# Kernel optimization log

Hardware: AMD Instinct MI355X
Metric: run time of the kernel (lower is better)

## Reference

```python
import jax, jax.numpy as jnp
import numpy as np

GROUPS = 32
EPS = 1e-3  # keras GroupNormalization default epsilon


def setup_inputs() -> dict:
    key = jax.random.key(0)
    ks = jax.random.split(key, 7)
    B, H, W, C = 16, 32, 32, 512
    inputs = jax.random.normal(ks[0], (B, H, W, C), dtype=jnp.float32)
    gamma = jnp.ones((C,), dtype=jnp.float32)
    beta = jnp.zeros((C,), dtype=jnp.float32)
    # EinsumDense 'bhwc,cae->bhwae', output last dims (C,3), bias axes 'ae'
    W_qkv = jax.random.normal(ks[1], (C, C, 3), dtype=jnp.float32) / np.sqrt(C)
    b_qkv = jnp.zeros((C, 3), dtype=jnp.float32)
    # EinsumDense 'bhwc,cd->bhwd', bias axes 'd'
    W_out = jax.random.normal(ks[2], (C, C), dtype=jnp.float32) / np.sqrt(C)
    b_out = jnp.zeros((C,), dtype=jnp.float32)
    return {
        "inputs": inputs,
        "gamma": gamma,
        "beta": beta,
        "W_qkv": W_qkv,
        "b_qkv": b_qkv,
        "W_out": W_out,
        "b_out": b_out,
    }


def group_norm(x, gamma, beta):
    B, H, W, C = x.shape
    g = GROUPS
    xr = x.reshape(B, H, W, g, C // g)
    mean = jnp.mean(xr, axis=(1, 2, 4), keepdims=True)
    var = jnp.var(xr, axis=(1, 2, 4), keepdims=True)
    xn = (xr - mean) * jax.lax.rsqrt(var + EPS)
    return xn.reshape(B, H, W, C) * gamma + beta


def reference(inputs, gamma, beta, W_qkv, b_qkv, W_out, b_out):
    B, H, W, C = inputs.shape
    scale = C ** (-0.5)
    x = group_norm(inputs, gamma, beta)
    # QKV projection: bhwc,cae->bhwae  (+ bias over 'ae')
    qkv = jnp.einsum("bhwc,cae->bhwae", x, W_qkv) + b_qkv
    q, k, v = qkv[..., 0], qkv[..., 1], qkv[..., 2]  # each [B,H,W,C]
    # full spatial attention: [B,H,W,H,W]
    attn = jnp.einsum("bhwc,btlc->bhwtl", q, k) * scale
    attn = attn.reshape(B, H, W, H * W)
    attn = jax.nn.softmax(attn, axis=-1)
    attn = attn.reshape(B, H, W, H, W)
    out = jnp.einsum("bhwtl,btlc->bhwc", attn, v)
    out = jnp.einsum("bhwc,cd->bhwd", out, W_out) + b_out
    return inputs + out
```

## Files before the change

### kernel.cpp

```cpp
#include <hip/hip_runtime.h>
#include <hip/hip_bf16.h>

#define NB    16
#define SP    1024
#define NC    512
#define NG    32
#define MTOT  (NB*SP)
#define EPSV  1e-3f
#define SCALE 0.04419417382415922f

using f32x4   = __attribute__((ext_vector_type(4))) float;
using short8  = __attribute__((ext_vector_type(8))) short;
using short4v = __attribute__((ext_vector_type(4))) short;
using bf16x8v = __attribute__((ext_vector_type(8))) __bf16;

__device__ __forceinline__ unsigned short f2bf(float f) {
  union { float f; unsigned int u; } x; x.f = f;
  unsigned int u = x.u;
  unsigned int r = (u + 0x7FFFu + ((u >> 16) & 1u)) >> 16;
  return (unsigned short)r;
}
__device__ __forceinline__ float bf2f(unsigned short b) {
  union { unsigned int u; float f; } x; x.u = ((unsigned int)b) << 16;
  return x.f;
}

#define GLOAD_LDS16(g, l)                                                     \
  __builtin_amdgcn_global_load_lds(                                           \
      (const __attribute__((address_space(1))) void*)(g),                     \
      (__attribute__((address_space(3))) void*)(l), 16, 0, 0)

__global__ __launch_bounds__(256) void gn_stats_k(const float* __restrict__ x,
                                                  float2* __restrict__ stats) {
  int bg = blockIdx.x;
  int b = bg >> 5, g = bg & 31;
  int tid = threadIdx.x;
  int c = tid & 15, s0 = tid >> 4;
  const float* base = x + (long)b * SP * NC + g * 16 + c;
  float s = 0.f, ss = 0.f;
  for (int sp = s0; sp < SP; sp += 16) {
    float v = base[(long)sp * NC];
    s += v; ss += v * v;
  }
  for (int o = 32; o > 0; o >>= 1) { s += __shfl_xor(s, o); ss += __shfl_xor(ss, o); }
  __shared__ float rs[4], rss[4];
  int lane = tid & 63, wv = tid >> 6;
  if (lane == 0) { rs[wv] = s; rss[wv] = ss; }
  __syncthreads();
  if (tid == 0) {
    float S = rs[0] + rs[1] + rs[2] + rs[3];
    float SS = rss[0] + rss[1] + rss[2] + rss[3];
    float mean = S * (1.f / 16384.f);
    float var  = SS * (1.f / 16384.f) - mean * mean;
    stats[bg] = make_float2(mean, rsqrtf(var + EPSV));
  }
}

__global__ __launch_bounds__(256) void gn_apply_k(const float* __restrict__ x,
                                                  const float2* __restrict__ stats,
                                                  const float* __restrict__ gamma,
                                                  const float* __restrict__ beta,
                                                  unsigned short* __restrict__ xn) {
  long t = (long)blockIdx.x * 256 + threadIdx.x;
  long base = t * 8;
  int c = (int)(base & 511);
  int b = (int)(base >> 19);
  float2 st = stats[b * NG + (c >> 4)];
  f32x4 v0 = *reinterpret_cast<const f32x4*>(x + base);
  f32x4 v1 = *reinterpret_cast<const f32x4*>(x + base + 4);
  f32x4 g0 = *reinterpret_cast<const f32x4*>(gamma + c);
  f32x4 g1 = *reinterpret_cast<const f32x4*>(gamma + c + 4);
  f32x4 b0 = *reinterpret_cast<const f32x4*>(beta + c);
  f32x4 b1 = *reinterpret_cast<const f32x4*>(beta + c + 4);
  short8 o;
  #pragma unroll
  for (int q = 0; q < 4; ++q) {
    float sc = st.y * g0[q];
    o[q] = (short)f2bf(v0[q] * sc + (b0[q] - st.x * sc));
  }
  #pragma unroll
  for (int q = 0; q < 4; ++q) {
    float sc = st.y * g1[q];
    o[q + 4] = (short)f2bf(v1[q] * sc + (b1[q] - st.x * sc));
  }
  *reinterpret_cast<short8*>(xn + base) = o;
}

__global__ __launch_bounds__(256) void pack_wqkv_k(const float* __restrict__ W,
                                                   const float* __restrict__ bq,
                                                   unsigned short* __restrict__ Wp,
                                                   float* __restrict__ bp) {
  int idx = blockIdx.x * 256 + threadIdx.x;
  int n = idx >> 9, c = idx & 511;
  int e = n >> 9, a = n & 511;
  Wp[idx] = f2bf(W[((long)c * 512 + a) * 3 + e]);
  if (idx < 1536) {
    int e2 = idx >> 9, a2 = idx & 511;
    bp[idx] = bq[a2 * 3 + e2];
  }
}

__global__ __launch_bounds__(256) void pack_wout_k(const float* __restrict__ W,
                                                   unsigned short* __restrict__ Wp) {
  int idx = blockIdx.x * 256 + threadIdx.x;
  int n = idx >> 9, c = idx & 511;
  Wp[idx] = f2bf(W[(long)c * 512 + n]);
}

__global__ void transpose_v_k(const unsigned short* __restrict__ qkv,
                              unsigned short* __restrict__ vT) {
  __shared__ unsigned short t[32][33];
  int bs = blockIdx.x, bc = blockIdx.y, b = blockIdx.z;
  int tx = threadIdx.x, ty = threadIdx.y;
  #pragma unroll
  for (int k = 0; k < 4; ++k) {
    int s = bs * 32 + ty + k * 8, c = bc * 32 + tx;
    t[ty + k * 8][tx] = qkv[((long)b * SP + s) * 1536 + 1024 + c];
  }
  __syncthreads();
  #pragma unroll
  for (int k = 0; k < 4; ++k) {
    int c = bc * 32 + ty + k * 8, s = bs * 32 + tx;
    vT[((long)b * NC + c) * SP + s] = t[tx][ty + k * 8];
  }
}

__global__ __launch_bounds__(256) void softmax_k(unsigned short* __restrict__ S) {
  long row = blockIdx.x;
  unsigned short* r = S + row * 1024;
  int tid = threadIdx.x, lane = tid & 63, wv = tid >> 6;
  short4v raw = *reinterpret_cast<const short4v*>(r + tid * 4);
  float v[4];
  #pragma unroll
  for (int q = 0; q < 4; ++q) v[q] = bf2f((unsigned short)raw[q]);
  float m = fmaxf(fmaxf(v[0], v[1]), fmaxf(v[2], v[3]));
  for (int o = 32; o > 0; o >>= 1) m = fmaxf(m, __shfl_xor(m, o));
  __shared__ float wm[4], ws[4];
  if (lane == 0) wm[wv] = m;
  __syncthreads();
  float rmax = fmaxf(fmaxf(wm[0], wm[1]), fmaxf(wm[2], wm[3]));
  float e[4]; float ssum = 0.f;
  #pragma unroll
  for (int q = 0; q < 4; ++q) { e[q] = __expf(v[q] - rmax); ssum += e[q]; }
  for (int o = 32; o > 0; o >>= 1) ssum += __shfl_xor(ssum, o);
  if (lane == 0) ws[wv] = ssum;
  __syncthreads();
  float inv = 1.f / (ws[0] + ws[1] + ws[2] + ws[3]);
  short4v pv;
  #pragma unroll
  for (int q = 0; q < 4; ++q) pv[q] = (short)f2bf(e[q] * inv);
  *reinterpret_cast<short4v*>(r + tid * 4) = pv;
}

template <int EPI>
__global__ __launch_bounds__(512, 2) void gemm8(
    const unsigned short* __restrict__ Ap, long strideA, int lda,
    const unsigned short* __restrict__ Bp, long strideB, int ldb,
    void* __restrict__ Op, long strideO, int ldo,
    const float* __restrict__ bias, const float* __restrict__ residual,
    int K, float scale) {
  constexpr int SLOT = 24576;
  extern __shared__ unsigned char smem[];
  const int tid = threadIdx.x;
  const int lane = tid & 63, wv = tid >> 6;
  const int wm2 = wv >> 2, wn4 = wv & 3;

  const int nwg  = gridDim.x * gridDim.y;
  const int flat = blockIdx.y * gridDim.x + blockIdx.x;
  const int w    = (flat & 7) * (nwg >> 3) + (flat >> 3);
  const int bn = (w % gridDim.x) * 256;
  const int bm = (w / gridDim.x) * 128;
  const int z = blockIdx.z;
  const unsigned short* Ag = Ap + (long)z * strideA;
  const unsigned short* Bg = Bp + (long)z * strideB;

  long offA;
  { int sid = tid, sr = sid >> 3, sl = (sid & 7) ^ (sr & 7);
    offA = (long)(bm + sr * 2 + (sl >> 2)) * lda + (sl & 3) * 8; }
  long offB0, offB1;
  { int sid = tid, sr = sid >> 3, sl = (sid & 7) ^ (sr & 7);
    offB0 = (long)(bn + sr * 2 + (sl >> 2)) * ldb + (sl & 3) * 8;
    sid = 512 + tid; sr = sid >> 3; sl = (sid & 7) ^ (sr & 7);
    offB1 = (long)(bn + sr * 2 + (sl >> 2)) * ldb + (sl & 3) * 8; }
  const int ldsA_off  = wv * 1024;
  const int ldsB0_off = 8192 + wv * 1024;
  const int ldsB1_off = 16384 + wv * 1024;

  int aoff[4], boff[4];
  #pragma unroll
  for (int i = 0; i < 4; ++i) {
    int r = wm2 * 64 + i * 16 + (lane & 15);
    int sr = r >> 1, sl = ((r & 1) * 4 + (lane >> 4)) ^ (sr & 7);
    aoff[i] = sr * 128 + sl * 16;
  }
  #pragma unroll
  for (int j = 0; j < 4; ++j) {
    int r = wn4 * 64 + j * 16 + (lane & 15);
    int sr = r >> 1, sl = ((r & 1) * 4 + (lane >> 4)) ^ (sr & 7);
    boff[j] = 8192 + sr * 128 + sl * 16;
  }

#define STAGE(tt, sb) do { long kt = (long)(tt) * 32;                 \
    GLOAD_LDS16(Ag + offA + kt,  smem + (sb) + ldsA_off);             \
    GLOAD_LDS16(Bg + offB0 + kt, smem + (sb) + ldsB0_off);            \
    GLOAD_LDS16(Bg + offB1 + kt, smem + (sb) + ldsB1_off); } while (0)

#define READS(av, bv, sa) do {                                        \
    _Pragma("unroll")                                                 \
    for (int i = 0; i < 4; ++i)                                       \
      av[i] = *reinterpret_cast<const short8*>((sa) + aoff[i]);       \
    _Pragma("unroll")                                                 \
    for (int j = 0; j < 4; ++j)                                       \
      bv[j] = *reinterpret_cast<const short8*>((sa) + boff[j]); } while (0)

#define MFMA16(av, bv) do {                                           \
    _Pragma("unroll")                                                 \
    for (int i = 0; i < 4; ++i)                                       \
      _Pragma("unroll")                                               \
      for (int j = 0; j < 4; ++j)                                     \
        acc[i][j] = __builtin_amdgcn_mfma_f32_16x16x32_bf16(          \
            __builtin_bit_cast(bf16x8v, av[i]),                       \
            __builtin_bit_cast(bf16x8v, bv[j]), acc[i][j], 0, 0, 0);  \
    } while (0)

  const int NT = K >> 5;
  #pragma unroll
  for (int t = 0; t < 3; ++t)
    if (t < NT) STAGE(t, t * SLOT);
  asm volatile("s_waitcnt vmcnt(3)" ::: "memory");
  __builtin_amdgcn_s_barrier();
  __builtin_amdgcn_sched_barrier(0);

  short8 a0[4], b0[4], a1[4], b1[4];
  READS(a0, b0, smem);
  f32x4 acc[4][4] = {};

  for (int t = 0; t < NT; t += 2) {
    if (t + 3 < NT) STAGE(t + 3, ((t + 3) & 3) * SLOT);
    if (t + 1 < NT) { const unsigned char* sa = smem + ((t + 1) & 3) * SLOT; READS(a1, b1, sa); }
    __builtin_amdgcn_sched_barrier(0);
    __builtin_amdgcn_s_setprio(1);
    MFMA16(a0, b0);
    __builtin_amdgcn_s_setprio(0);
    __builtin_amdgcn_sched_barrier(0);
    if (t + 3 < NT) asm volatile("s_waitcnt vmcnt(3)" ::: "memory");
    else            asm volatile("s_waitcnt vmcnt(0)" ::: "memory");
    __builtin_amdgcn_s_barrier();
    __builtin_amdgcn_sched_barrier(0);

    if (t + 1 < NT) {
      if (t + 4 < NT) STAGE(t + 4, ((t + 4) & 3) * SLOT);
      if (t + 2 < NT) { const unsigned char* sa = smem + ((t + 2) & 3) * SLOT; READS(a0, b0, sa); }
      __builtin_amdgcn_sched_barrier(0);
      __builtin_amdgcn_s_setprio(1);
      MFMA16(a1, b1);
      __builtin_amdgcn_s_setprio(0);
      __builtin_amdgcn_sched_barrier(0);
      if (t + 4 < NT) asm volatile("s_waitcnt vmcnt(3)" ::: "memory");
      else            asm volatile("s_waitcnt vmcnt(0)" ::: "memory");
      __builtin_amdgcn_s_barrier();
      __builtin_amdgcn_sched_barrier(0);
    }
  }
#undef STAGE
#undef READS
#undef MFMA16

  const int colb = bn + wn4 * 64 + (lane & 15);
  const int rowb = bm + wm2 * 64 + (lane >> 4) * 4;
  #pragma unroll
  for (int i = 0; i < 4; ++i) {
    #pragma unroll
    for (int r = 0; r < 4; ++r) {
      int rowg = rowb + i * 16 + r;
      #pragma unroll
      for (int j = 0; j < 4; ++j) {
        int colg = colb + j * 16;
        float v = acc[i][j][r];
        if (EPI == 0) {
          v += bias[colg];
          ((unsigned short*)Op)[(long)z * strideO + (long)rowg * ldo + colg] = f2bf(v);
        } else if (EPI == 2) {
          ((unsigned short*)Op)[(long)z * strideO + (long)rowg * ldo + colg] = f2bf(v * scale);
        } else {
          v += bias[colg] + residual[(long)rowg * ldo + colg];
          ((float*)Op)[(long)rowg * ldo + colg] = v;
        }
      }
    }
  }
}

extern "C" void kernel_launch(void* const* d_in, const int* in_sizes, int n_in,
                              void* d_out, int out_size, void* d_ws, size_t ws_size,
                              hipStream_t stream) {
  const float* x     = (const float*)d_in[0];
  const float* gamma = (const float*)d_in[1];
  const float* beta  = (const float*)d_in[2];
  const float* Wqkv  = (const float*)d_in[3];
  const float* bqkv  = (const float*)d_in[4];
  const float* Wout  = (const float*)d_in[5];
  const float* bout  = (const float*)d_in[6];
  float* out = (float*)d_out;

  char* ws = (char*)d_ws;
  float2*         stats = (float2*)(ws + 0);
  unsigned short* wqkvP = (unsigned short*)(ws + 4096);
  float*          bqP   = (float*)(ws + 1576960);
  unsigned short* woutT = (unsigned short*)(ws + 1583104);
  unsigned short* qkv   = (unsigned short*)(ws + 2107392);
  unsigned short* vT    = (unsigned short*)(ws + 52439040);
  unsigned short* Sbuf  = (unsigned short*)(ws + 69216256);
  unsigned short* attn  = (unsigned short*)(ws + 136325120);
  unsigned short* xn    = (unsigned short*)(ws + 153102336);

  (void)hipFuncSetAttribute((const void*)gemm8<0>,
        hipFuncAttributeMaxDynamicSharedMemorySize, 98304);
  (void)hipFuncSetAttribute((const void*)gemm8<2>,
        hipFuncAttributeMaxDynamicSharedMemorySize, 98304);
  (void)hipFuncSetAttribute((const void*)gemm8<3>,
        hipFuncAttributeMaxDynamicSharedMemorySize, 98304);

  gn_stats_k<<<512, 256, 0, stream>>>(x, stats);
  gn_apply_k<<<4096, 256, 0, stream>>>(x, stats, gamma, beta, xn);
  pack_wqkv_k<<<3072, 256, 0, stream>>>(Wqkv, bqkv, wqkvP, bqP);
  pack_wout_k<<<1024, 256, 0, stream>>>(Wout, woutT);

  gemm8<0><<<dim3(6, 128, 1), 512, 98304, stream>>>(
      xn, 0L, NC, wqkvP, 0L, NC, qkv, 0L, 1536,
      bqP, nullptr, NC, 1.f);

  transpose_v_k<<<dim3(32, 16, 16), dim3(32, 8), 0, stream>>>(qkv, vT);

  gemm8<2><<<dim3(4, 8, 16), 512, 98304, stream>>>(
      qkv, (long)SP * 1536, 1536, qkv + 512, (long)SP * 1536, 1536,
      Sbuf, (long)SP * SP, SP, nullptr, nullptr, NC, SCALE);

  softmax_k<<<MTOT, 256, 0, stream>>>(Sbuf);

  gemm8<2><<<dim3(2, 8, 16), 512, 98304, stream>>>(
      Sbuf, (long)SP * SP, SP, vT, (long)NC * SP, SP,
      attn, (long)SP * NC, NC, nullptr, nullptr, SP, 1.f);

  gemm8<3><<<dim3(2, 128, 1), 512, 98304, stream>>>(
      attn, 0L, NC, woutT, 0L, NC, out, 0L, NC,
      bout, x, NC, 1.f);
}
```

Measured before the change: 280.3 us.

## Add 256x256-tile GEMM kernel for QKV projection and QK^T scores

Adds a gemm256 kernel that uses 256x256 output tiles (each wave computes 128x64) with four LDS slots of 32 KB and a prefetch depth of three stages. It replaces the 128x256 gemm8 for the QKV projection and the Q·K^T score GEMM, halving the grid. The goal is more data reuse per LDS load and higher MFMA density. The cost is 128 KB of LDS and twice the accumulator registers, which likely limits occupancy to one block per CU and leaves fewer workgroups to fill the machine.

```diff
diff --git a/kernel.cpp b/kernel.cpp
--- a/kernel.cpp
+++ b/kernel.cpp
@@ -153,6 +153,142 @@
 }
 
 template <int EPI>
+__global__ __launch_bounds__(512, 2) void gemm256(
+    const unsigned short* __restrict__ Ap, long strideA, int lda,
+    const unsigned short* __restrict__ Bp, long strideB, int ldb,
+    unsigned short* __restrict__ Op, long strideO, int ldo,
+    const float* __restrict__ bias, int K, float scale) {
+  constexpr int SLOT = 32768;
+  extern __shared__ unsigned char smem[];
+  const int tid = threadIdx.x;
+  const int lane = tid & 63, wv = tid >> 6;
+  const int wm2 = wv >> 2, wn4 = wv & 3;
+
+  const int nwg  = gridDim.x * gridDim.y;
+  const int flat = blockIdx.y * gridDim.x + blockIdx.x;
+  const int w    = (flat & 7) * (nwg >> 3) + (flat >> 3);
+  const int bn = (w % gridDim.x) * 256;
+  const int bm = (w / gridDim.x) * 256;
+  const int z = blockIdx.z;
+  const unsigned short* Ag = Ap + (long)z * strideA;
+  const unsigned short* Bg = Bp + (long)z * strideB;
+
+  long offA0, offA1, offB0, offB1;
+  { int sid = tid, sr = sid >> 3, sl = (sid & 7) ^ (sr & 7);
+    offA0 = (long)(bm + sr * 2 + (sl >> 2)) * lda + (sl & 3) * 8;
+    offB0 = (long)(bn + sr * 2 + (sl >> 2)) * ldb + (sl & 3) * 8;
+    sid = 512 + tid; sr = sid >> 3; sl = (sid & 7) ^ (sr & 7);
+    offA1 = (long)(bm + sr * 2 + (sl >> 2)) * lda + (sl & 3) * 8;
+    offB1 = (long)(bn + sr * 2 + (sl >> 2)) * ldb + (sl & 3) * 8; }
+  const int ldsA0 = wv * 1024;
+  const int ldsA1 = 8192  + wv * 1024;
+  const int ldsB0 = 16384 + wv * 1024;
+  const int ldsB1 = 24576 + wv * 1024;
+
+  int aoff[8], boff[4];
+  #pragma unroll
+  for (int i = 0; i < 8; ++i) {
+    int r = wm2 * 128 + i * 16 + (lane & 15);
+    int sr = r >> 1, sl = ((r & 1) * 4 + (lane >> 4)) ^ (sr & 7);
+    aoff[i] = sr * 128 + sl * 16;
+  }
+  #pragma unroll
+  for (int j = 0; j < 4; ++j) {
+    int r = wn4 * 64 + j * 16 + (lane & 15);
+    int sr = r >> 1, sl = ((r & 1) * 4 + (lane >> 4)) ^ (sr & 7);
+    boff[j] = 16384 + sr * 128 + sl * 16;
+  }
+
+#define STAGE6(tt, sb) do { long kt = (long)(tt) * 32;                \
+    GLOAD_LDS16(Ag + offA0 + kt, smem + (sb) + ldsA0);                \
+    GLOAD_LDS16(Ag + offA1 + kt, smem + (sb) + ldsA1);                \
+    GLOAD_LDS16(Bg + offB0 + kt, smem + (sb) + ldsB0);                \
+    GLOAD_LDS16(Bg + offB1 + kt, smem + (sb) + ldsB1); } while (0)
+
+#define READS6(av, bv, sa) do {                                       \
+    _Pragma("unroll")                                                 \
+    for (int i = 0; i < 8; ++i)                                       \
+      av[i] = *reinterpret_cast<const short8*>((sa) + aoff[i]);       \
+    _Pragma("unroll")                                                 \
+    for (int j = 0; j < 4; ++j)                                       \
+      bv[j] = *reinterpret_cast<const short8*>((sa) + boff[j]); } while (0)
+
+#define MFMA32(av, bv) do {                                           \
+    _Pragma("unroll")                                                 \
+    for (int i = 0; i < 8; ++i)                                       \
+      _Pragma("unroll")                                               \
+      for (int j = 0; j < 4; ++j)                                     \
+        acc[i][j] = __builtin_amdgcn_mfma_f32_16x16x32_bf16(          \
+            __builtin_bit_cast(bf16x8v, av[i]),                       \
+            __builtin_bit_cast(bf16x8v, bv[j]), acc[i][j], 0, 0, 0);  \
+    } while (0)
+
+  const int NT = K >> 5;
+  #pragma unroll
+  for (int t = 0; t < 3; ++t)
+    STAGE6(t, t * SLOT);
+  asm volatile("s_waitcnt vmcnt(4)" ::: "memory");
+  __builtin_amdgcn_s_barrier();
+  __builtin_amdgcn_sched_barrier(0);
+
+  short8 a0[8], b0[4], a1[8], b1[4];
+  READS6(a0, b0, smem);
+  f32x4 acc[8][4] = {};
+
+  for (int t = 0; t < NT; t += 2) {
+    if (t + 3 < NT) STAGE6(t + 3, ((t + 3) & 3) * SLOT);
+    if (t + 1 < NT) { const unsigned char* sa = smem + ((t + 1) & 3) * SLOT; READS6(a1, b1, sa); }
+    __builtin_amdgcn_sched_barrier(0);
+    __builtin_amdgcn_s_setprio(1);
+    MFMA32(a0, b0);
+    __builtin_amdgcn_s_setprio(0);
+    __builtin_amdgcn_sched_barrier(0);
+    if (t + 3 < NT) asm volatile("s_waitcnt vmcnt(4)" ::: "memory");
+    else            asm volatile("s_waitcnt vmcnt(0)" ::: "memory");
+    __builtin_amdgcn_s_barrier();
+    __builtin_amdgcn_sched_barrier(0);
+
+    if (t + 1 < NT) {
+      if (t + 4 < NT) STAGE6(t + 4, ((t + 4) & 3) * SLOT);
+      if (t + 2 < NT) { const unsigned char* sa = smem + ((t + 2) & 3) * SLOT; READS6(a0, b0, sa); }
+      __builtin_amdgcn_sched_barrier(0);
+      __builtin_amdgcn_s_setprio(1);
+      MFMA32(a1, b1);
+      __builtin_amdgcn_s_setprio(0);
+      __builtin_amdgcn_sched_barrier(0);
+      if (t + 4 < NT) asm volatile("s_waitcnt vmcnt(4)" ::: "memory");
+      else            asm volatile("s_waitcnt vmcnt(0)" ::: "memory");
+      __builtin_amdgcn_s_barrier();
+      __builtin_amdgcn_sched_barrier(0);
+    }
+  }
+#undef STAGE6
+#undef READS6
+#undef MFMA32
+
+  const int colb = bn + wn4 * 64 + (lane & 15);
+  const int rowb = bm + wm2 * 128 + (lane >> 4) * 4;
+  #pragma unroll
+  for (int i = 0; i < 8; ++i) {
+    #pragma unroll
+    for (int r = 0; r < 4; ++r) {
+      long rowg = rowb + i * 16 + r;
+      #pragma unroll
+      for (int j = 0; j < 4; ++j) {
+        int colg = colb + j * 16;
+        float v = acc[i][j][r];
+        if (EPI == 0) {
+          v += bias[colg];
+          Op[(long)z * strideO + rowg * ldo + colg] = f2bf(v);
+        } else {
+          Op[(long)z * strideO + rowg * ldo + colg] = f2bf(v * scale);
+        }
+      }
+    }
+  }
+}
+
+template <int EPI>
 __global__ __launch_bounds__(512, 2) void gemm8(
     const unsigned short* __restrict__ Ap, long strideA, int lda,
     const unsigned short* __restrict__ Bp, long strideB, int ldb,
@@ -277,10 +413,7 @@
       for (int j = 0; j < 4; ++j) {
         int colg = colb + j * 16;
         float v = acc[i][j][r];
-        if (EPI == 0) {
-          v += bias[colg];
-          ((unsigned short*)Op)[(long)z * strideO + (long)rowg * ldo + colg] = f2bf(v);
-        } else if (EPI == 2) {
+        if (EPI == 2) {
           ((unsigned short*)Op)[(long)z * strideO + (long)rowg * ldo + colg] = f2bf(v * scale);
         } else {
           v += bias[colg] + residual[(long)rowg * ldo + colg];
@@ -314,8 +447,10 @@
   unsigned short* attn  = (unsigned short*)(ws + 136325120);
   unsigned short* xn    = (unsigned short*)(ws + 153102336);
 
-  (void)hipFuncSetAttribute((const void*)gemm8<0>,
-        hipFuncAttributeMaxDynamicSharedMemorySize, 98304);
+  (void)hipFuncSetAttribute((const void*)gemm256<0>,
+        hipFuncAttributeMaxDynamicSharedMemorySize, 131072);
+  (void)hipFuncSetAttribute((const void*)gemm256<2>,
+        hipFuncAttributeMaxDynamicSharedMemorySize, 131072);
   (void)hipFuncSetAttribute((const void*)gemm8<2>,
         hipFuncAttributeMaxDynamicSharedMemorySize, 98304);
   (void)hipFuncSetAttribute((const void*)gemm8<3>,
@@ -326,15 +461,15 @@
   pack_wqkv_k<<<3072, 256, 0, stream>>>(Wqkv, bqkv, wqkvP, bqP);
   pack_wout_k<<<1024, 256, 0, stream>>>(Wout, woutT);
 
-  gemm8<0><<<dim3(6, 128, 1), 512, 98304, stream>>>(
+  gemm256<0><<<dim3(6, 64, 1), 512, 131072, stream>>>(
       xn, 0L, NC, wqkvP, 0L, NC, qkv, 0L, 1536,
-      bqP, nullptr, NC, 1.f);
+      bqP, NC, 1.f);
 
   transpose_v_k<<<dim3(32, 16, 16), dim3(32, 8), 0, stream>>>(qkv, vT);
 
-  gemm8<2><<<dim3(4, 8, 16), 512, 98304, stream>>>(
+  gemm256<2><<<dim3(4, 4, 16), 512, 131072, stream>>>(
       qkv, (long)SP * 1536, 1536, qkv + 512, (long)SP * 1536, 1536,
-      Sbuf, (long)SP * SP, SP, nullptr, nullptr, NC, SCALE);
+      Sbuf, (long)SP * SP, SP, nullptr, NC, SCALE);
 
   softmax_k<<<MTOT, 256, 0, stream>>>(Sbuf);
 
```

Result: faster. 273.0 us (-2.6%).
